# Optimization experiments

Hardware: AMD Instinct MI355X
Metric: run time of the kernel (lower is better)

The kernel has to match this reference:

```python
import jax, jax.numpy as jnp
import numpy as np

N_NODES = 50000
N_EDGES = 800000
IN_F = 256
OUT_F = 128
ALPHA = 0.2  # LeakyReLU negative slope


def setup_inputs() -> dict:
    key = jax.random.key(0)
    k_h, k_row, k_col, k_W, k_a = jax.random.split(key, 5)
    h = jax.random.normal(k_h, (N_NODES, IN_F), dtype=jnp.float32)
    row = jax.random.randint(k_row, (N_EDGES,), 0, N_NODES)
    # Guarantee every node appears as a destination so unique(dst) == arange(N)
    col = jnp.concatenate([
        jnp.arange(N_NODES),
        jax.random.randint(k_col, (N_EDGES - N_NODES,), 0, N_NODES),
    ])
    adj = jnp.stack([row, col]).astype(jnp.int64)
    # Xavier-uniform-ish params (gain 1.414)
    lim_W = 1.414 * np.sqrt(6.0 / (IN_F + OUT_F))
    W = jax.random.uniform(k_W, (IN_F, OUT_F), minval=-lim_W, maxval=lim_W, dtype=jnp.float32)
    lim_a = 1.414 * np.sqrt(6.0 / (2 * OUT_F + 1))
    a = jax.random.uniform(k_a, (2 * OUT_F, 1), minval=-lim_a, maxval=lim_a, dtype=jnp.float32)
    return {"h": h, "adj": adj, "W": W, "a": a}


def reference(h, adj, W, a):
    N = h.shape[0]
    self_loops = jnp.arange(N)  # == unique(adj[1]) by input construction
    row = jnp.concatenate([adj[0], self_loops])  # [E_total]
    col = jnp.concatenate([adj[1], self_loops])  # [E_total]

    Wh = h @ W                                    # [N, OUT_F]
    s_src = (Wh @ a[:OUT_F]).squeeze(-1)          # [N] (Wh1)
    s_dst = (Wh @ a[OUT_F:]).squeeze(-1)          # [N] (Wh2)

    e = jax.nn.leaky_relu(s_dst[col] + s_src[row], negative_slope=ALPHA)  # [E_total]

    # segment softmax over destination nodes
    e_max = jax.ops.segment_max(e, col, num_segments=N)
    ex = jnp.exp(e - e_max[col])
    denom = jax.ops.segment_sum(ex, col, num_segments=N)
    att = ex / denom[col]                         # [E_total]

    h_prime = jax.ops.segment_sum(Wh[row] * att[:, None], col, num_segments=N)  # [N, OUT_F]
    return jax.nn.elu(h_prime)  # concat=True
```

## Files before the change

### kernel.cpp

```cpp
#include <hip/hip_runtime.h>
#include <math.h>

#define N_NODES 50000
#define N_EDGES 800000
#define IN_F 256
#define OUT_F 128
#define ALPHA 0.2f
#define SLOT_CAP 64

#define NODE_BLOCKS ((N_NODES + 255) / 256)
#define GEMM_WAVES ((N_NODES + 15) / 16)
#define GEMM_BLOCKS ((GEMM_WAVES + 3) / 4)
#define EDGE_BLOCKS ((N_EDGES + 255) / 256)

typedef short bf16x8 __attribute__((ext_vector_type(8)));
typedef float f32x4  __attribute__((ext_vector_type(4)));

static __device__ __forceinline__ unsigned short f2bf(float f) {
    unsigned int u = __float_as_uint(f);
    u += 0x7FFFu + ((u >> 16) & 1u);
    return (unsigned short)(u >> 16);
}
static __device__ __forceinline__ float bf2f(unsigned int u16) {
    return __uint_as_float(u16 << 16);
}

__global__ __launch_bounds__(256) void k_prep(const float* __restrict__ W,
                                              const float* __restrict__ a,
                                              int* __restrict__ cnt,
                                              float* __restrict__ Wa,
                                              unsigned short* __restrict__ WbT) {
    const int b = blockIdx.x, t = threadIdx.x;
    if (b < NODE_BLOCKS) {
        int i = b * 256 + t;
        if (i < N_NODES) cnt[i] = 0;
    } else if (b == NODE_BLOCKS) {
        const int k = t;
        const float4* wr  = (const float4*)(W + (size_t)k * OUT_F);
        const float4* av1 = (const float4*)a;
        const float4* av2 = (const float4*)(a + OUT_F);
        float s1 = 0.0f, s2 = 0.0f;
#pragma unroll 8
        for (int i = 0; i < OUT_F / 4; ++i) {
            float4 w = wr[i], x = av1[i], y = av2[i];
            s1 = fmaf(w.x, x.x, fmaf(w.y, x.y, fmaf(w.z, x.z, fmaf(w.w, x.w, s1))));
            s2 = fmaf(w.x, y.x, fmaf(w.y, y.y, fmaf(w.z, y.z, fmaf(w.w, y.w, s2))));
        }
        Wa[k] = s1;
        Wa[IN_F + k] = s2;
    } else {
        const int n = b - (NODE_BLOCKS + 1);
        WbT[(size_t)n * IN_F + t] = f2bf(W[(size_t)t * OUT_F + n]);
    }
}

__global__ __launch_bounds__(256) void k_main(const float* __restrict__ h,
                                              const unsigned short* __restrict__ WbT,
                                              const float* __restrict__ Wa,
                                              const int* __restrict__ adj,
                                              unsigned short* __restrict__ Whb,
                                              float* __restrict__ s_src,
                                              float* __restrict__ s_dst,
                                              int* __restrict__ cnt,
                                              int* __restrict__ slots) {
    if (blockIdx.x >= GEMM_BLOCKS) {
        const int e = (blockIdx.x - GEMM_BLOCKS) * 256 + threadIdx.x;
        if (e < N_EDGES) {
            const int src = adj[e];
            const int dst = adj[N_EDGES + e];
            const int p = atomicAdd(&cnt[dst], 1);
            if (p < SLOT_CAP) slots[(size_t)dst * SLOT_CAP + p] = src;
        }
        return;
    }
    const int wid = blockIdx.x * 4 + (threadIdx.x >> 6);
    if (wid >= GEMM_WAVES) return;
    const int lane = threadIdx.x & 63;
    const int m = lane & 15, grp = lane >> 4;
    const int row = wid * 16 + m;

    f32x4 acc[8];
#pragma unroll
    for (int nt = 0; nt < 8; ++nt) acc[nt] = (f32x4){0.f, 0.f, 0.f, 0.f};
    float sp1 = 0.0f, sp2 = 0.0f;

    const float* hrow = h + (size_t)row * IN_F;
    for (int kt = 0; kt < 8; ++kt) {
        const int k0 = kt * 32 + grp * 8;
        const float4* hp = (const float4*)(hrow + k0);
        float4 x0 = hp[0], x1 = hp[1];
        const float4* wap1 = (const float4*)(Wa + k0);
        const float4* wap2 = (const float4*)(Wa + IN_F + k0);
        float4 a0 = wap1[0], a1 = wap1[1];
        float4 b0 = wap2[0], b1 = wap2[1];
        sp1 = fmaf(x0.x, a0.x, fmaf(x0.y, a0.y, fmaf(x0.z, a0.z, fmaf(x0.w, a0.w, sp1))));
        sp1 = fmaf(x1.x, a1.x, fmaf(x1.y, a1.y, fmaf(x1.z, a1.z, fmaf(x1.w, a1.w, sp1))));
        sp2 = fmaf(x0.x, b0.x, fmaf(x0.y, b0.y, fmaf(x0.z, b0.z, fmaf(x0.w, b0.w, sp2))));
        sp2 = fmaf(x1.x, b1.x, fmaf(x1.y, b1.y, fmaf(x1.z, b1.z, fmaf(x1.w, b1.w, sp2))));
        bf16x8 hf;
        hf[0] = (short)f2bf(x0.x); hf[1] = (short)f2bf(x0.y);
        hf[2] = (short)f2bf(x0.z); hf[3] = (short)f2bf(x0.w);
        hf[4] = (short)f2bf(x1.x); hf[5] = (short)f2bf(x1.y);
        hf[6] = (short)f2bf(x1.z); hf[7] = (short)f2bf(x1.w);
#pragma unroll
        for (int nt = 0; nt < 8; ++nt) {
            bf16x8 wf = *(const bf16x8*)(WbT + (size_t)(nt * 16 + m) * IN_F + k0);
            acc[nt] = __builtin_amdgcn_mfma_f32_16x16x32_bf16(wf, hf, acc[nt], 0, 0, 0);
        }
    }

    float t1 = sp1, t2 = sp2;
    t1 += __shfl_xor(t1, 16); t1 += __shfl_xor(t1, 32);
    t2 += __shfl_xor(t2, 16); t2 += __shfl_xor(t2, 32);
    if (grp == 0) { s_src[row] = t1; s_dst[row] = t2; }

    unsigned short* orow = Whb + (size_t)row * OUT_F;
#pragma unroll
    for (int nt = 0; nt < 8; ++nt) {
        f32x4 v = acc[nt];
        ushort4 pk;
        pk.x = f2bf(v[0]); pk.y = f2bf(v[1]);
        pk.z = f2bf(v[2]); pk.w = f2bf(v[3]);
        *(ushort4*)(orow + nt * 16 + grp * 4) = pk;
    }
}

__global__ __launch_bounds__(256) void k_gather(const unsigned short* __restrict__ Whb,
                                                const int* __restrict__ cnt,
                                                const int* __restrict__ slots,
                                                const float* __restrict__ s_src,
                                                const float* __restrict__ s_dst,
                                                float* __restrict__ out) {
    const int wid  = (blockIdx.x * blockDim.x + threadIdx.x) >> 6;
    const int lane = threadIdx.x & 63;
    const int grp  = lane >> 4;
    const int l    = lane & 15;
    const int node = wid * 4 + grp;
    if (node >= N_NODES) return;

    const float sd = s_dst[node];
    float s0 = sd + s_src[node];
    float lr0 = (s0 > 0.0f) ? s0 : ALPHA * s0;
    float x0 = __expf(lr0);
    uint4 w0 = ((const uint4*)(Whb + (size_t)node * OUT_F))[l];
    float a0 = x0 * bf2f(w0.x & 0xFFFFu);
    float a1 = x0 * bf2f(w0.x >> 16);
    float a2 = x0 * bf2f(w0.y & 0xFFFFu);
    float a3 = x0 * bf2f(w0.y >> 16);
    float a4 = x0 * bf2f(w0.z & 0xFFFFu);
    float a5 = x0 * bf2f(w0.z >> 16);
    float a6 = x0 * bf2f(w0.w & 0xFFFFu);
    float a7 = x0 * bf2f(w0.w >> 16);
    float dsum = x0;

    const int deg = min(cnt[node], SLOT_CAP);
    const int* __restrict__ srow = slots + (size_t)node * SLOT_CAP;
    const int lb = grp * 16;

    for (int base = 0; base < deg; base += 16) {
        const int nh  = min(16, deg - base);
        const int myi = base + l;
        int   sv = 0;
        float xv = 0.0f;
        if (myi < deg) {
            sv = srow[myi];
            float s = sd + s_src[sv];
            float lr = (s > 0.0f) ? s : ALPHA * s;
            xv = __expf(lr);
        }
        float t = xv;
        t += __shfl_xor(t, 1);
        t += __shfl_xor(t, 2);
        t += __shfl_xor(t, 4);
        t += __shfl_xor(t, 8);
        dsum += t;
#pragma unroll 2
        for (int i = 0; i < nh; ++i) {
            const int   src = __shfl(sv, lb + i);
            const float x   = __shfl(xv, lb + i);
            const uint4 wv = ((const uint4*)(Whb + (size_t)src * OUT_F))[l];
            a0 = fmaf(x, bf2f(wv.x & 0xFFFFu), a0);
            a1 = fmaf(x, bf2f(wv.x >> 16), a1);
            a2 = fmaf(x, bf2f(wv.y & 0xFFFFu), a2);
            a3 = fmaf(x, bf2f(wv.y >> 16), a3);
            a4 = fmaf(x, bf2f(wv.z & 0xFFFFu), a4);
            a5 = fmaf(x, bf2f(wv.z >> 16), a5);
            a6 = fmaf(x, bf2f(wv.w & 0xFFFFu), a6);
            a7 = fmaf(x, bf2f(wv.w >> 16), a7);
        }
    }

    const float inv = 1.0f / dsum;
    float4 o0, o1;
    o0.x = a0 * inv; o0.y = a1 * inv; o0.z = a2 * inv; o0.w = a3 * inv;
    o1.x = a4 * inv; o1.y = a5 * inv; o1.z = a6 * inv; o1.w = a7 * inv;
    o0.x = (o0.x > 0.0f) ? o0.x : expm1f(o0.x);
    o0.y = (o0.y > 0.0f) ? o0.y : expm1f(o0.y);
    o0.z = (o0.z > 0.0f) ? o0.z : expm1f(o0.z);
    o0.w = (o0.w > 0.0f) ? o0.w : expm1f(o0.w);
    o1.x = (o1.x > 0.0f) ? o1.x : expm1f(o1.x);
    o1.y = (o1.y > 0.0f) ? o1.y : expm1f(o1.y);
    o1.z = (o1.z > 0.0f) ? o1.z : expm1f(o1.z);
    o1.w = (o1.w > 0.0f) ? o1.w : expm1f(o1.w);
    float4* op = (float4*)(out + (size_t)node * OUT_F + l * 8);
    op[0] = o0;
    op[1] = o1;
}

extern "C" void kernel_launch(void* const* d_in, const int* in_sizes, int n_in,
                              void* d_out, int out_size, void* d_ws, size_t ws_size,
                              hipStream_t stream) {
    const float* h   = (const float*)d_in[0];
    const int*   adj = (const int*)d_in[1];
    const float* W   = (const float*)d_in[2];
    const float* a   = (const float*)d_in[3];
    float* out = (float*)d_out;

    char* ws = (char*)d_ws;
    const size_t SZ_WHB = (size_t)N_NODES * OUT_F * 2;
    const size_t SZ_N   = 200704;
    unsigned short* Whb = (unsigned short*)(ws);
    float* s_src   = (float*)(ws + SZ_WHB);
    float* s_dst   = (float*)(ws + SZ_WHB + SZ_N);
    int*   cnt     = (int*)  (ws + SZ_WHB + 2 * SZ_N);
    float* Wa      = (float*)(ws + SZ_WHB + 3 * SZ_N);
    unsigned short* WbT = (unsigned short*)(ws + SZ_WHB + 3 * SZ_N + 2048);
    int*   slots   = (int*)  (ws + SZ_WHB + 3 * SZ_N + 2048 + 65536);

    (void)in_sizes; (void)n_in; (void)out_size; (void)ws_size;

    k_prep  <<<NODE_BLOCKS + 1 + OUT_F, 256, 0, stream>>>(W, a, cnt, Wa, WbT);
    k_main  <<<GEMM_BLOCKS + EDGE_BLOCKS, 256, 0, stream>>>(h, WbT, Wa, adj, Whb,
                                                            s_src, s_dst, cnt, slots);
    k_gather<<<(N_NODES / 4 * 64) / 256, 256, 0, stream>>>(Whb, cnt, slots,
                                                           s_src, s_dst, out);
}
```

Before: 199.6 us.

## Pad per-node counters to 64 bytes and unroll gather by four edges

Each node's atomic degree counter now sits in its own 64-byte stride, so concurrent atomics on neighbouring destinations no longer share a cache line. The gather loop drops the shuffle-based broadcast of source indices and attention weights. Instead every lane reads four slot indices with one int4 load, issues four independent Whb row loads, and computes the exponentials redundantly, giving more memory-level parallelism. The cost is a 16x larger counter array to zero, reads of slot entries past deg that are clamped and masked to zero, and duplicated exp work across lanes.

```diff
diff --git a/kernel.cpp b/kernel.cpp
--- a/kernel.cpp
+++ b/kernel.cpp
@@ -7,6 +7,7 @@
 #define OUT_F 128
 #define ALPHA 0.2f
 #define SLOT_CAP 64
+#define CNT_STRIDE 16
 
 #define NODE_BLOCKS ((N_NODES + 255) / 256)
 #define GEMM_WAVES ((N_NODES + 15) / 16)
@@ -33,7 +34,11 @@
     const int b = blockIdx.x, t = threadIdx.x;
     if (b < NODE_BLOCKS) {
         int i = b * 256 + t;
-        if (i < N_NODES) cnt[i] = 0;
+        if (i < N_NODES) {
+            int4 z = make_int4(0, 0, 0, 0);
+            int4* p = (int4*)(cnt + (size_t)i * CNT_STRIDE);
+            p[0] = z; p[1] = z; p[2] = z; p[3] = z;
+        }
     } else if (b == NODE_BLOCKS) {
         const int k = t;
         const float4* wr  = (const float4*)(W + (size_t)k * OUT_F);
@@ -68,7 +73,7 @@
         if (e < N_EDGES) {
             const int src = adj[e];
             const int dst = adj[N_EDGES + e];
-            const int p = atomicAdd(&cnt[dst], 1);
+            const int p = atomicAdd(&cnt[(size_t)dst * CNT_STRIDE], 1);
             if (p < SLOT_CAP) slots[(size_t)dst * SLOT_CAP + p] = src;
         }
         return;
@@ -153,41 +158,63 @@
     float a7 = x0 * bf2f(w0.w >> 16);
     float dsum = x0;
 
-    const int deg = min(cnt[node], SLOT_CAP);
+    const int deg = min(cnt[(size_t)node * CNT_STRIDE], SLOT_CAP);
     const int* __restrict__ srow = slots + (size_t)node * SLOT_CAP;
-    const int lb = grp * 16;
-
-    for (int base = 0; base < deg; base += 16) {
-        const int nh  = min(16, deg - base);
-        const int myi = base + l;
-        int   sv = 0;
-        float xv = 0.0f;
-        if (myi < deg) {
-            sv = srow[myi];
-            float s = sd + s_src[sv];
-            float lr = (s > 0.0f) ? s : ALPHA * s;
-            xv = __expf(lr);
-        }
-        float t = xv;
-        t += __shfl_xor(t, 1);
-        t += __shfl_xor(t, 2);
-        t += __shfl_xor(t, 4);
-        t += __shfl_xor(t, 8);
-        dsum += t;
-#pragma unroll 2
-        for (int i = 0; i < nh; ++i) {
-            const int   src = __shfl(sv, lb + i);
-            const float x   = __shfl(xv, lb + i);
-            const uint4 wv = ((const uint4*)(Whb + (size_t)src * OUT_F))[l];
-            a0 = fmaf(x, bf2f(wv.x & 0xFFFFu), a0);
-            a1 = fmaf(x, bf2f(wv.x >> 16), a1);
-            a2 = fmaf(x, bf2f(wv.y & 0xFFFFu), a2);
-            a3 = fmaf(x, bf2f(wv.y >> 16), a3);
-            a4 = fmaf(x, bf2f(wv.z & 0xFFFFu), a4);
-            a5 = fmaf(x, bf2f(wv.z >> 16), a5);
-            a6 = fmaf(x, bf2f(wv.w & 0xFFFFu), a6);
-            a7 = fmaf(x, bf2f(wv.w >> 16), a7);
-        }
+
+    for (int i = 0; i < deg; i += 4) {
+        const int4 q = *(const int4*)(srow + i);
+        const unsigned su0 = min((unsigned)q.x, N_NODES - 1u);
+        const unsigned su1 = min((unsigned)q.y, N_NODES - 1u);
+        const unsigned su2 = min((unsigned)q.z, N_NODES - 1u);
+        const unsigned su3 = min((unsigned)q.w, N_NODES - 1u);
+        const float e0 = sd + s_src[su0];
+        const float e1 = sd + s_src[su1];
+        const float e2 = sd + s_src[su2];
+        const float e3 = sd + s_src[su3];
+        const uint4 v0 = ((const uint4*)(Whb + (size_t)su0 * OUT_F))[l];
+        const uint4 v1 = ((const uint4*)(Whb + (size_t)su1 * OUT_F))[l];
+        const uint4 v2 = ((const uint4*)(Whb + (size_t)su2 * OUT_F))[l];
+        const uint4 v3 = ((const uint4*)(Whb + (size_t)su3 * OUT_F))[l];
+        float x_0 = __expf((e0 > 0.0f) ? e0 : ALPHA * e0);
+        float x_1 = __expf((e1 > 0.0f) ? e1 : ALPHA * e1);
+        float x_2 = __expf((e2 > 0.0f) ? e2 : ALPHA * e2);
+        float x_3 = __expf((e3 > 0.0f) ? e3 : ALPHA * e3);
+        x_1 = (i + 1 < deg) ? x_1 : 0.0f;
+        x_2 = (i + 2 < deg) ? x_2 : 0.0f;
+        x_3 = (i + 3 < deg) ? x_3 : 0.0f;
+        dsum += x_0 + x_1 + x_2 + x_3;
+        a0 = fmaf(x_0, bf2f(v0.x & 0xFFFFu), a0);
+        a1 = fmaf(x_0, bf2f(v0.x >> 16), a1);
+        a2 = fmaf(x_0, bf2f(v0.y & 0xFFFFu), a2);
+        a3 = fmaf(x_0, bf2f(v0.y >> 16), a3);
+        a4 = fmaf(x_0, bf2f(v0.z & 0xFFFFu), a4);
+        a5 = fmaf(x_0, bf2f(v0.z >> 16), a5);
+        a6 = fmaf(x_0, bf2f(v0.w & 0xFFFFu), a6);
+        a7 = fmaf(x_0, bf2f(v0.w >> 16), a7);
+        a0 = fmaf(x_1, bf2f(v1.x & 0xFFFFu), a0);
+        a1 = fmaf(x_1, bf2f(v1.x >> 16), a1);
+        a2 = fmaf(x_1, bf2f(v1.y & 0xFFFFu), a2);
+        a3 = fmaf(x_1, bf2f(v1.y >> 16), a3);
+        a4 = fmaf(x_1, bf2f(v1.z & 0xFFFFu), a4);
+        a5 = fmaf(x_1, bf2f(v1.z >> 16), a5);
+        a6 = fmaf(x_1, bf2f(v1.w & 0xFFFFu), a6);
+        a7 = fmaf(x_1, bf2f(v1.w >> 16), a7);
+        a0 = fmaf(x_2, bf2f(v2.x & 0xFFFFu), a0);
+        a1 = fmaf(x_2, bf2f(v2.x >> 16), a1);
+        a2 = fmaf(x_2, bf2f(v2.y & 0xFFFFu), a2);
+        a3 = fmaf(x_2, bf2f(v2.y >> 16), a3);
+        a4 = fmaf(x_2, bf2f(v2.z & 0xFFFFu), a4);
+        a5 = fmaf(x_2, bf2f(v2.z >> 16), a5);
+        a6 = fmaf(x_2, bf2f(v2.w & 0xFFFFu), a6);
+        a7 = fmaf(x_2, bf2f(v2.w >> 16), a7);
+        a0 = fmaf(x_3, bf2f(v3.x & 0xFFFFu), a0);
+        a1 = fmaf(x_3, bf2f(v3.x >> 16), a1);
+        a2 = fmaf(x_3, bf2f(v3.y & 0xFFFFu), a2);
+        a3 = fmaf(x_3, bf2f(v3.y >> 16), a3);
+        a4 = fmaf(x_3, bf2f(v3.z & 0xFFFFu), a4);
+        a5 = fmaf(x_3, bf2f(v3.z >> 16), a5);
+        a6 = fmaf(x_3, bf2f(v3.w & 0xFFFFu), a6);
+        a7 = fmaf(x_3, bf2f(v3.w >> 16), a7);
     }
 
     const float inv = 1.0f / dsum;
@@ -219,13 +246,14 @@
     char* ws = (char*)d_ws;
     const size_t SZ_WHB = (size_t)N_NODES * OUT_F * 2;
     const size_t SZ_N   = 200704;
+    const size_t SZ_CNT = (size_t)N_NODES * CNT_STRIDE * 4;
     unsigned short* Whb = (unsigned short*)(ws);
     float* s_src   = (float*)(ws + SZ_WHB);
     float* s_dst   = (float*)(ws + SZ_WHB + SZ_N);
     int*   cnt     = (int*)  (ws + SZ_WHB + 2 * SZ_N);
-    float* Wa      = (float*)(ws + SZ_WHB + 3 * SZ_N);
-    unsigned short* WbT = (unsigned short*)(ws + SZ_WHB + 3 * SZ_N + 2048);
-    int*   slots   = (int*)  (ws + SZ_WHB + 3 * SZ_N + 2048 + 65536);
+    float* Wa      = (float*)(ws + SZ_WHB + 2 * SZ_N + SZ_CNT);
+    unsigned short* WbT = (unsigned short*)(ws + SZ_WHB + 2 * SZ_N + SZ_CNT + 2048);
+    int*   slots   = (int*)  (ws + SZ_WHB + 2 * SZ_N + SZ_CNT + 2048 + 65536);
 
     (void)in_sizes; (void)n_in; (void)out_size; (void)ws_size;
 
```

Result: no change. 197.2 us (-1.2%).
